# Performance work log

Hardware: AMD Instinct MI355X
Metric: run time of the kernel (lower is better)

The kernel has to match this reference:

```python
import jax, jax.numpy as jnp
import numpy as np


def _splat(img, sx, sy, w):
    """One bilinear-gaussian corner splat (scatter-add).
    img: (N,C,H,W); sx,sy,w: (N,1,H,W) integer-valued float shifts + weight.
    Returns (img_warp, one_warp) each (N,C,H,W).
    """
    N, C, H, W = img.shape
    ix = sx.astype(jnp.int32) + jnp.arange(H, dtype=jnp.int32)[None, None, :, None]
    iy = sy.astype(jnp.int32) + jnp.arange(W, dtype=jnp.int32)[None, None, None, :]
    mask = (ix >= 0) & (ix < H) & (iy >= 0) & (iy < W)          # (N,1,H,W)
    ixc = jnp.clip(ix, 0, H - 1)
    iyc = jnp.clip(iy, 0, W - 1)
    nb = jnp.arange(N, dtype=jnp.int32)[:, None, None, None]
    cb = jnp.arange(C, dtype=jnp.int32)[None, :, None, None]
    ids = ((nb * C + cb) * H + ixc) * W + iyc                   # (N,C,H,W)
    ids = jnp.broadcast_to(ids, (N, C, H, W)).reshape(-1)
    wv = jnp.where(mask, w, 0.0)                                # invalid -> 0 contribution
    vals = jnp.broadcast_to(img * wv, (N, C, H, W)).reshape(-1)
    wflat = jnp.broadcast_to(wv, (N, C, H, W)).reshape(-1)
    img_warp = jnp.zeros(N * C * H * W, img.dtype).at[ids].add(vals)
    one_warp = jnp.zeros(N * C * H * W, img.dtype).at[ids].add(wflat)
    return img_warp.reshape(N, C, H, W), one_warp.reshape(N, C, H, W)


def setup_inputs() -> dict:
    key = jax.random.key(0)
    k1, k2 = jax.random.split(key)
    N, C, H, W = 4, 128, 216, 384
    img = jax.random.normal(k1, (N, C, H, W), dtype=jnp.float32)
    # flow displacements of a few pixels magnitude (realistic optical flow)
    flo = jax.random.normal(k2, (N, 2, H, W), dtype=jnp.float32) * 8.0
    return {"img": img, "flo": flo}


def reference(img, flo):
    # y shifts rows (H axis), x shifts cols (W axis), matching the torch code
    y = flo[:, 0:1]    # (N,1,H,W)
    x = flo[:, 1:2]
    x1 = jnp.floor(x); x2 = x1 + 1.0
    y1 = jnp.floor(y); y2 = y1 + 1.0
    w11 = jnp.exp(-((x - x1) ** 2 + (y - y1) ** 2))
    w12 = jnp.exp(-((x - x1) ** 2 + (y - y2) ** 2))
    w21 = jnp.exp(-((x - x2) ** 2 + (y - y1) ** 2))
    w22 = jnp.exp(-((x - x2) ** 2 + (y - y2) ** 2))
    img11, o11 = _splat(img, x1, y1, w11)
    img12, o12 = _splat(img, x1, y2, w12)
    img21, o21 = _splat(img, x2, y1, w21)
    img22, o22 = _splat(img, x2, y2, w22)
    imgw = img11 + img12 + img21 + img22
    o = o11 + o12 + o21 + o22
    return imgw, o
```

## Files before the change

### kernel.cpp

```cpp
#include <hip/hip_runtime.h>


constexpr int N_ = 4, C_ = 128, H_ = 216, W_ = 384;
constexpr int HW    = H_ * W_;
constexpr int TOTAL = N_ * C_ * HW;
constexpr int PIX   = N_ * HW;
constexpr int SCAN_BLOCKS = PIX / 256;

constexpr size_t OFF_IMGT   = 0;
constexpr size_t OFF_OUTT   = (size_t)TOTAL;
constexpr size_t OFF_COUNTS = 2ull * TOTAL;
constexpr size_t OFF_CURSOR = OFF_COUNTS + PIX;
constexpr size_t OFF_OFFS   = OFF_CURSOR + PIX;
constexpr size_t OFF_BS     = OFF_OFFS + PIX;
constexpr size_t OFF_ONES   = OFF_BS + 4096;
constexpr size_t OFF_ES     = OFF_ONES + PIX;
constexpr size_t OFF_EW     = OFF_ES + 4ull * PIX;
constexpr size_t WS_ELEMS   = OFF_EW + 4ull * PIX;
constexpr size_t WS_BYTES   = WS_ELEMS * 4;

__device__ inline void corner_math(float fx, float fy, int& ifx, int& ify,
                                   float& ex0, float& ex1, float& ey0, float& ey1) {
    float fx1 = floorf(fx), fy1 = floorf(fy);
    float dx = fx - fx1, dy = fy - fy1;
    ifx = (int)fx1; ify = (int)fy1;
    ex0 = __expf(-dx * dx);
    ex1 = __expf(-(dx - 1.f) * (dx - 1.f));
    ey0 = __expf(-dy * dy);
    ey1 = __expf(-(dy - 1.f) * (dy - 1.f));
}

__global__ __launch_bounds__(256) void transpose_fwd_k(const float* __restrict__ img,
                                                       float* __restrict__ imgT) {
    __shared__ float tile[32][33];
    int n   = blockIdx.z;
    int hw0 = blockIdx.x * 32;
    int c0  = blockIdx.y * 32;
    const float* src = img  + (size_t)n * C_ * HW;
    float*       dst = imgT + (size_t)n * HW * C_;
    int tx = threadIdx.x, ty = threadIdx.y;
#pragma unroll
    for (int r = 0; r < 32; r += 8)
        tile[ty + r][tx] = src[(size_t)(c0 + ty + r) * HW + hw0 + tx];
    __syncthreads();
#pragma unroll
    for (int r = 0; r < 32; r += 8)
        dst[(size_t)(hw0 + ty + r) * C_ + c0 + tx] = tile[tx][ty + r];
}

__global__ __launch_bounds__(256) void count_k(const float* __restrict__ flo,
                                               unsigned int* __restrict__ counts) {
    int idx = blockIdx.x * 256 + threadIdx.x;
    if (idx >= PIX) return;
    int s = idx % HW, n = idx / HW;
    int h = s / W_, w = s % W_;
    float fy = flo[(n * 2 + 0) * HW + s];
    float fx = flo[(n * 2 + 1) * HW + s];
    int ifx, ify; float ex0, ex1, ey0, ey1;
    corner_math(fx, fy, ifx, ify, ex0, ex1, ey0, ey1);
    int ix = h + ifx, iy = w + ify;
    unsigned int* base = counts + (size_t)n * HW;
    bool bx0 = (unsigned)ix       < (unsigned)H_;
    bool bx1 = (unsigned)(ix + 1) < (unsigned)H_;
    bool by0 = (unsigned)iy       < (unsigned)W_;
    bool by1 = (unsigned)(iy + 1) < (unsigned)W_;
    if (bx0 && by0) atomicAdd(base + ix * W_ + iy, 1u);
    if (bx0 && by1) atomicAdd(base + ix * W_ + iy + 1, 1u);
    if (bx1 && by0) atomicAdd(base + (ix + 1) * W_ + iy, 1u);
    if (bx1 && by1) atomicAdd(base + (ix + 1) * W_ + iy + 1, 1u);
}

__global__ __launch_bounds__(256) void scan_local_k(const unsigned int* __restrict__ counts,
                                                    unsigned int* __restrict__ offs,
                                                    unsigned int* __restrict__ bs) {
    __shared__ unsigned int tmp[256];
    int tid = threadIdx.x;
    int i = blockIdx.x * 256 + tid;
    unsigned int v = counts[i];
    tmp[tid] = v;
    __syncthreads();
    for (int off = 1; off < 256; off <<= 1) {
        unsigned int t = (tid >= off) ? tmp[tid - off] : 0u;
        __syncthreads();
        tmp[tid] += t;
        __syncthreads();
    }
    offs[i] = tmp[tid] - v;
    if (tid == 255) bs[blockIdx.x] = tmp[tid];
}

__global__ __launch_bounds__(256) void scan_bs_k(unsigned int* __restrict__ bs) {
    __shared__ unsigned int tmp[256];
    constexpr int IT = 6;
    int tid = threadIdx.x;
    unsigned int v[IT]; unsigned int sum = 0;
#pragma unroll
    for (int i = 0; i < IT; ++i) {
        int j = tid * IT + i;
        v[i] = (j < SCAN_BLOCKS) ? bs[j] : 0u;
        sum += v[i];
    }
    tmp[tid] = sum;
    __syncthreads();
    for (int off = 1; off < 256; off <<= 1) {
        unsigned int t = (tid >= off) ? tmp[tid - off] : 0u;
        __syncthreads();
        tmp[tid] += t;
        __syncthreads();
    }
    unsigned int run = tmp[tid] - sum;
#pragma unroll
    for (int i = 0; i < IT; ++i) {
        int j = tid * IT + i;
        if (j < SCAN_BLOCKS) { unsigned int old = v[i]; bs[j] = run; run += old; }
    }
}

__global__ __launch_bounds__(256) void scan_add_k(unsigned int* __restrict__ offs,
                                                  const unsigned int* __restrict__ bs) {
    int i = blockIdx.x * 256 + threadIdx.x;
    offs[i] += bs[blockIdx.x];
}

__global__ __launch_bounds__(256) void fill_k(const float* __restrict__ flo,
                                              const unsigned int* __restrict__ offs,
                                              unsigned int* __restrict__ cursor,
                                              unsigned int* __restrict__ entry_s,
                                              float* __restrict__ entry_w) {
    int idx = blockIdx.x * 256 + threadIdx.x;
    if (idx >= PIX) return;
    int s = idx % HW, n = idx / HW;
    int h = s / W_, w = s % W_;
    float fy = flo[(n * 2 + 0) * HW + s];
    float fx = flo[(n * 2 + 1) * HW + s];
    int ifx, ify; float ex0, ex1, ey0, ey1;
    corner_math(fx, fy, ifx, ify, ex0, ex1, ey0, ey1);
    int ix = h + ifx, iy = w + ify;
    bool bx[2] = { (unsigned)ix < (unsigned)H_, (unsigned)(ix + 1) < (unsigned)H_ };
    bool by[2] = { (unsigned)iy < (unsigned)W_, (unsigned)(iy + 1) < (unsigned)W_ };
    float exw[2] = { ex0, ex1 }, eyw[2] = { ey0, ey1 };
#pragma unroll
    for (int a = 0; a < 2; ++a) {
#pragma unroll
        for (int b = 0; b < 2; ++b) {
            if (bx[a] && by[b]) {
                int t = n * HW + (ix + a) * W_ + (iy + b);
                unsigned int slot = atomicAdd(cursor + t, 1u);
                unsigned int e = offs[t] + slot;
                entry_s[e] = (unsigned int)s;
                entry_w[e] = exw[a] * eyw[b];
            }
        }
    }
}

__global__ __launch_bounds__(256) void gather_k(const float* __restrict__ imgT,
                                                const unsigned int* __restrict__ counts,
                                                const unsigned int* __restrict__ offs,
                                                const unsigned int* __restrict__ entry_s,
                                                const float* __restrict__ entry_w,
                                                float* __restrict__ outT,
                                                float* __restrict__ ones_plane) {
    int pl = threadIdx.x >> 5;
    int cg = threadIdx.x & 31;
    int t  = blockIdx.x * 8 + pl;
    int n = t / HW, p = t % HW;
    unsigned int k   = counts[t];
    unsigned int off = offs[t];
    float4 acc = make_float4(0.f, 0.f, 0.f, 0.f);
    float wsum = 0.f;
    const float4* srcBase = (const float4*)(imgT + (size_t)n * HW * C_);
    for (unsigned int j = 0; j < k; ++j) {
        unsigned int s = entry_s[off + j];
        float wgt     = entry_w[off + j];
        float4 v = srcBase[(size_t)s * (C_ / 4) + cg];
        acc.x += wgt * v.x; acc.y += wgt * v.y;
        acc.z += wgt * v.z; acc.w += wgt * v.w;
        wsum += wgt;
    }
    ((float4*)(outT + ((size_t)n * HW + p) * C_))[cg] = acc;
    if (cg == 0) ones_plane[t] = wsum;
}

__global__ __launch_bounds__(256) void transpose_back_k(const float* __restrict__ outT,
                                                        float* __restrict__ out) {
    __shared__ float tile[32][33];
    int n   = blockIdx.z;
    int hw0 = blockIdx.x * 32;
    int c0  = blockIdx.y * 32;
    const float* src = outT + (size_t)n * HW * C_;
    float*       dst = out  + (size_t)n * C_ * HW;
    int tx = threadIdx.x, ty = threadIdx.y;
#pragma unroll
    for (int r = 0; r < 32; r += 8)
        tile[ty + r][tx] = src[(size_t)(hw0 + ty + r) * C_ + c0 + tx];
    __syncthreads();
#pragma unroll
    for (int r = 0; r < 32; r += 8)
        dst[(size_t)(c0 + ty + r) * HW + hw0 + tx] = tile[tx][ty + r];
}

__global__ __launch_bounds__(256) void ones_bcast_k(const float* __restrict__ ones_plane,
                                                    float* __restrict__ out_ones) {
    constexpr int HW4 = HW / 4;
    int idx = blockIdx.x * 256 + threadIdx.x;
    int p  = idx % HW4;
    int cn = idx / HW4;
    int c  = cn % C_;
    int n  = cn / C_;
    const float4* src = (const float4*)(ones_plane + (size_t)n * HW);
    float4*       dst = (float4*)(out_ones + ((size_t)n * C_ + c) * HW);
    dst[p] = src[p];
}

__global__ __launch_bounds__(256) void fb_ones_scatter_k(const float* __restrict__ flo,
                                                         float* __restrict__ out_ones) {
    int idx = blockIdx.x * 256 + threadIdx.x;
    if (idx >= PIX) return;
    int w = idx % W_; int hn = idx / W_; int h = hn % H_; int n = hn / H_;
    float fy = flo[(n * 2 + 0) * HW + h * W_ + w];
    float fx = flo[(n * 2 + 1) * HW + h * W_ + w];
    int ifx, ify; float ex0, ex1, ey0, ey1;
    corner_math(fx, fy, ifx, ify, ex0, ex1, ey0, ey1);
    int ix = h + ifx, iy = w + ify;
    float* plane = out_ones + (size_t)n * C_ * HW;
    if ((unsigned)ix < (unsigned)H_ && (unsigned)iy < (unsigned)W_) atomicAdd(plane + ix * W_ + iy, ex0 * ey0);
    if ((unsigned)ix < (unsigned)H_ && (unsigned)(iy+1) < (unsigned)W_) atomicAdd(plane + ix * W_ + iy + 1, ex0 * ey1);
    if ((unsigned)(ix+1) < (unsigned)H_ && (unsigned)iy < (unsigned)W_) atomicAdd(plane + (ix+1) * W_ + iy, ex1 * ey0);
    if ((unsigned)(ix+1) < (unsigned)H_ && (unsigned)(iy+1) < (unsigned)W_) atomicAdd(plane + (ix+1) * W_ + iy + 1, ex1 * ey1);
}

__global__ __launch_bounds__(256) void fb_img_scatter_k(const float* __restrict__ img,
                                                        const float* __restrict__ flo,
                                                        float* __restrict__ out_img) {
    int idx = blockIdx.x * 256 + threadIdx.x;
    if (idx >= TOTAL) return;
    int w = idx % W_; int rem = idx / W_; int h = rem % H_; rem /= H_;
    int c = rem % C_; int n = rem / C_;
    float fy = flo[(n * 2 + 0) * HW + h * W_ + w];
    float fx = flo[(n * 2 + 1) * HW + h * W_ + w];
    int ifx, ify; float ex0, ex1, ey0, ey1;
    corner_math(fx, fy, ifx, ify, ex0, ex1, ey0, ey1);
    int ix = h + ifx, iy = w + ify;
    float v = img[idx];
    float* plane = out_img + (size_t)(n * C_ + c) * HW;
    if ((unsigned)ix < (unsigned)H_ && (unsigned)iy < (unsigned)W_) atomicAdd(plane + ix * W_ + iy, v * ex0 * ey0);
    if ((unsigned)ix < (unsigned)H_ && (unsigned)(iy+1) < (unsigned)W_) atomicAdd(plane + ix * W_ + iy + 1, v * ex0 * ey1);
    if ((unsigned)(ix+1) < (unsigned)H_ && (unsigned)iy < (unsigned)W_) atomicAdd(plane + (ix+1) * W_ + iy, v * ex1 * ey0);
    if ((unsigned)(ix+1) < (unsigned)H_ && (unsigned)(iy+1) < (unsigned)W_) atomicAdd(plane + (ix+1) * W_ + iy + 1, v * ex1 * ey1);
}

__global__ __launch_bounds__(256) void fb_ones_bcast_k(float* __restrict__ out_ones) {
    constexpr int HW4 = HW / 4;
    constexpr int TOT = N_ * (C_ - 1) * HW4;
    int idx = blockIdx.x * 256 + threadIdx.x;
    if (idx >= TOT) return;
    int p = idx % HW4; int cn = idx / HW4;
    int c = 1 + cn % (C_ - 1); int n = cn / (C_ - 1);
    const float4* src = (const float4*)(out_ones + (size_t)n * C_ * HW);
    float4*       dst = (float4*)(out_ones + ((size_t)n * C_ + c) * HW);
    dst[p] = src[p];
}

extern "C" void kernel_launch(void* const* d_in, const int* in_sizes, int n_in,
                              void* d_out, int out_size, void* d_ws, size_t ws_size,
                              hipStream_t stream) {
    const float* img = (const float*)d_in[0];
    const float* flo = (const float*)d_in[1];
    float* out      = (float*)d_out;
    float* out_img  = out;
    float* out_ones = out + (size_t)TOTAL;

    if (ws_size < WS_BYTES) {
        hipMemsetAsync(out_img, 0, (size_t)TOTAL * sizeof(float), stream);
        for (int n = 0; n < N_; ++n)
            hipMemsetAsync(out_ones + (size_t)n * C_ * HW, 0, HW * sizeof(float), stream);
        fb_ones_scatter_k<<<(PIX + 255) / 256, 256, 0, stream>>>(flo, out_ones);
        fb_img_scatter_k<<<(TOTAL + 255) / 256, 256, 0, stream>>>(img, flo, out_img);
        fb_ones_bcast_k<<<(N_ * (C_ - 1) * (HW / 4) + 255) / 256, 256, 0, stream>>>(out_ones);
        return;
    }

    float* ws = (float*)d_ws;
    float*        imgT    = ws + OFF_IMGT;
    float*        outT    = ws + OFF_OUTT;
    unsigned int* counts  = (unsigned int*)(ws + OFF_COUNTS);
    unsigned int* cursor  = (unsigned int*)(ws + OFF_CURSOR);
    unsigned int* offs    = (unsigned int*)(ws + OFF_OFFS);
    unsigned int* bs      = (unsigned int*)(ws + OFF_BS);
    float*        ones_pl = ws + OFF_ONES;
    unsigned int* entry_s = (unsigned int*)(ws + OFF_ES);
    float*        entry_w = ws + OFF_EW;

    hipMemsetAsync(counts, 0, 2ull * PIX * sizeof(unsigned int), stream);

    dim3 tb(32, 8);
    transpose_fwd_k<<<dim3(HW / 32, C_ / 32, N_), tb, 0, stream>>>(img, imgT);
    count_k<<<SCAN_BLOCKS, 256, 0, stream>>>(flo, counts);
    scan_local_k<<<SCAN_BLOCKS, 256, 0, stream>>>(counts, offs, bs);
    scan_bs_k<<<1, 256, 0, stream>>>(bs);
    scan_add_k<<<SCAN_BLOCKS, 256, 0, stream>>>(offs, bs);
    fill_k<<<SCAN_BLOCKS, 256, 0, stream>>>(flo, offs, cursor, entry_s, entry_w);
    gather_k<<<PIX / 8, 256, 0, stream>>>(imgT, counts, offs, entry_s, entry_w, outT, ones_pl);
    transpose_back_k<<<dim3(HW / 32, C_ / 32, N_), tb, 0, stream>>>(outT, out_img);
    ones_bcast_k<<<(N_ * C_ * (HW / 4) + 255) / 256, 256, 0, stream>>>(ones_pl, out_ones);
}
```

Measured before the change: 778.1 us.

## Fuse gather with transpose-back and ones broadcast, pack entries, drop scan-add

The gather kernel now handles 64-pixel tiles. It accumulates channel-major results in registers, transposes them through an XOR-swizzled LDS tile, and writes the NCHW image output and the broadcast ones output directly. This removes the outT intermediate buffer, the transpose-back kernel and the ones broadcast kernel. Entry index and weight are packed into one uint2 array. The scan-add pass is folded into the consumers, which add the block sum on the fly. The gather loop is unrolled by two. The cost is a large 32 KB LDS tile per block, which may limit occupancy, plus higher register pressure from holding 8 float4 accumulators.

```diff
diff --git a/kernel.cpp b/kernel.cpp
--- a/kernel.cpp
+++ b/kernel.cpp
@@ -6,17 +6,16 @@
 constexpr int TOTAL = N_ * C_ * HW;
 constexpr int PIX   = N_ * HW;
 constexpr int SCAN_BLOCKS = PIX / 256;
+constexpr int PTILE = 64;
+constexpr int GATHER_BLOCKS = PIX / PTILE;
 
 constexpr size_t OFF_IMGT   = 0;
-constexpr size_t OFF_OUTT   = (size_t)TOTAL;
-constexpr size_t OFF_COUNTS = 2ull * TOTAL;
+constexpr size_t OFF_COUNTS = (size_t)TOTAL;
 constexpr size_t OFF_CURSOR = OFF_COUNTS + PIX;
 constexpr size_t OFF_OFFS   = OFF_CURSOR + PIX;
 constexpr size_t OFF_BS     = OFF_OFFS + PIX;
-constexpr size_t OFF_ONES   = OFF_BS + 4096;
-constexpr size_t OFF_ES     = OFF_ONES + PIX;
-constexpr size_t OFF_EW     = OFF_ES + 4ull * PIX;
-constexpr size_t WS_ELEMS   = OFF_EW + 4ull * PIX;
+constexpr size_t OFF_ENT    = OFF_BS + 4096;
+constexpr size_t WS_ELEMS   = OFF_ENT + 8ull * PIX;
 constexpr size_t WS_BYTES   = WS_ELEMS * 4;
 
 __device__ inline void corner_math(float fx, float fy, int& ifx, int& ify,
@@ -116,17 +115,11 @@
     }
 }
 
-__global__ __launch_bounds__(256) void scan_add_k(unsigned int* __restrict__ offs,
-                                                  const unsigned int* __restrict__ bs) {
-    int i = blockIdx.x * 256 + threadIdx.x;
-    offs[i] += bs[blockIdx.x];
-}
-
 __global__ __launch_bounds__(256) void fill_k(const float* __restrict__ flo,
                                               const unsigned int* __restrict__ offs,
+                                              const unsigned int* __restrict__ bs,
                                               unsigned int* __restrict__ cursor,
-                                              unsigned int* __restrict__ entry_s,
-                                              float* __restrict__ entry_w) {
+                                              uint2* __restrict__ entries) {
     int idx = blockIdx.x * 256 + threadIdx.x;
     if (idx >= PIX) return;
     int s = idx % HW, n = idx / HW;
@@ -146,71 +139,94 @@
             if (bx[a] && by[b]) {
                 int t = n * HW + (ix + a) * W_ + (iy + b);
                 unsigned int slot = atomicAdd(cursor + t, 1u);
-                unsigned int e = offs[t] + slot;
-                entry_s[e] = (unsigned int)s;
-                entry_w[e] = exw[a] * eyw[b];
+                unsigned int e = offs[t] + bs[t >> 8] + slot;
+                entries[e] = make_uint2((unsigned int)s,
+                                        __float_as_uint(exw[a] * eyw[b]));
             }
         }
     }
 }
 
-__global__ __launch_bounds__(256) void gather_k(const float* __restrict__ imgT,
-                                                const unsigned int* __restrict__ counts,
-                                                const unsigned int* __restrict__ offs,
-                                                const unsigned int* __restrict__ entry_s,
-                                                const float* __restrict__ entry_w,
-                                                float* __restrict__ outT,
-                                                float* __restrict__ ones_plane) {
-    int pl = threadIdx.x >> 5;
-    int cg = threadIdx.x & 31;
-    int t  = blockIdx.x * 8 + pl;
-    int n = t / HW, p = t % HW;
-    unsigned int k   = counts[t];
-    unsigned int off = offs[t];
-    float4 acc = make_float4(0.f, 0.f, 0.f, 0.f);
-    float wsum = 0.f;
+__global__ __launch_bounds__(256) void gather_fused_k(const float* __restrict__ imgT,
+                                                      const unsigned int* __restrict__ counts,
+                                                      const unsigned int* __restrict__ offs,
+                                                      const unsigned int* __restrict__ bs,
+                                                      const uint2* __restrict__ entries,
+                                                      float* __restrict__ out_img,
+                                                      float* __restrict__ out_ones) {
+    __shared__ float tile[C_ * PTILE];
+    __shared__ float wsum_lds[PTILE];
+
+    int tid = threadIdx.x;
+    int pl  = tid >> 5;
+    int cg  = tid & 31;
+    int bt  = blockIdx.x;
+    int n   = bt / (HW / PTILE);
+    int p0  = (bt % (HW / PTILE)) * PTILE;
     const float4* srcBase = (const float4*)(imgT + (size_t)n * HW * C_);
-    for (unsigned int j = 0; j < k; ++j) {
-        unsigned int s = entry_s[off + j];
-        float wgt     = entry_w[off + j];
-        float4 v = srcBase[(size_t)s * (C_ / 4) + cg];
-        acc.x += wgt * v.x; acc.y += wgt * v.y;
-        acc.z += wgt * v.z; acc.w += wgt * v.w;
-        wsum += wgt;
-    }
-    ((float4*)(outT + ((size_t)n * HW + p) * C_))[cg] = acc;
-    if (cg == 0) ones_plane[t] = wsum;
-}
-
-__global__ __launch_bounds__(256) void transpose_back_k(const float* __restrict__ outT,
-                                                        float* __restrict__ out) {
-    __shared__ float tile[32][33];
-    int n   = blockIdx.z;
-    int hw0 = blockIdx.x * 32;
-    int c0  = blockIdx.y * 32;
-    const float* src = outT + (size_t)n * HW * C_;
-    float*       dst = out  + (size_t)n * C_ * HW;
-    int tx = threadIdx.x, ty = threadIdx.y;
-#pragma unroll
-    for (int r = 0; r < 32; r += 8)
-        tile[ty + r][tx] = src[(size_t)(hw0 + ty + r) * C_ + c0 + tx];
+
+    float4 acc[8];
+    float  ws[8];
+#pragma unroll
+    for (int si = 0; si < 8; ++si) {
+        int p = si * 8 + pl;
+        int t = n * HW + p0 + p;
+        unsigned int k   = counts[t];
+        unsigned int off = offs[t] + bs[t >> 8];
+        float4 a = make_float4(0.f, 0.f, 0.f, 0.f);
+        float  w_s = 0.f;
+        unsigned int j = 0;
+        for (; j + 2 <= k; j += 2) {
+            uint2 e0 = entries[off + j];
+            uint2 e1 = entries[off + j + 1];
+            float w0 = __uint_as_float(e0.y);
+            float w1 = __uint_as_float(e1.y);
+            float4 v0 = srcBase[(size_t)e0.x * (C_ / 4) + cg];
+            float4 v1 = srcBase[(size_t)e1.x * (C_ / 4) + cg];
+            a.x = a.x + w0 * v0.x + w1 * v1.x;
+            a.y = a.y + w0 * v0.y + w1 * v1.y;
+            a.z = a.z + w0 * v0.z + w1 * v1.z;
+            a.w = a.w + w0 * v0.w + w1 * v1.w;
+            w_s = w_s + w0 + w1;
+        }
+        if (j < k) {
+            uint2 e0 = entries[off + j];
+            float w0 = __uint_as_float(e0.y);
+            float4 v0 = srcBase[(size_t)e0.x * (C_ / 4) + cg];
+            a.x += w0 * v0.x; a.y += w0 * v0.y;
+            a.z += w0 * v0.z; a.w += w0 * v0.w;
+            w_s += w0;
+        }
+        acc[si] = a; ws[si] = w_s;
+    }
+
+#pragma unroll
+    for (int si = 0; si < 8; ++si) {
+        int p  = si * 8 + pl;
+        if (cg == 0) wsum_lds[p] = ws[si];
+        int p4 = p >> 2, pr = p & 3;
+        float av[4] = { acc[si].x, acc[si].y, acc[si].z, acc[si].w };
+#pragma unroll
+        for (int jj = 0; jj < 4; ++jj) {
+            int c    = 4 * cg + jj;
+            int slot = p4 ^ ((c >> 2) & 15);
+            tile[c * PTILE + slot * 4 + pr] = av[jj];
+        }
+    }
     __syncthreads();
-#pragma unroll
-    for (int r = 0; r < 32; r += 8)
-        dst[(size_t)(c0 + ty + r) * HW + hw0 + tx] = tile[tx][ty + r];
-}
-
-__global__ __launch_bounds__(256) void ones_bcast_k(const float* __restrict__ ones_plane,
-                                                    float* __restrict__ out_ones) {
-    constexpr int HW4 = HW / 4;
-    int idx = blockIdx.x * 256 + threadIdx.x;
-    int p  = idx % HW4;
-    int cn = idx / HW4;
-    int c  = cn % C_;
-    int n  = cn / C_;
-    const float4* src = (const float4*)(ones_plane + (size_t)n * HW);
-    float4*       dst = (float4*)(out_ones + ((size_t)n * C_ + c) * HW);
-    dst[p] = src[p];
+
+    int p4    = tid & 15;
+    int cbase = tid >> 4;
+    float4 wv = ((const float4*)wsum_lds)[p4];
+#pragma unroll
+    for (int i = 0; i < 8; ++i) {
+        int c    = cbase + 16 * i;
+        int slot = p4 ^ ((c >> 2) & 15);
+        float4 v = *(const float4*)&tile[c * PTILE + slot * 4];
+        size_t o = ((size_t)(n * C_ + c)) * HW + p0 + p4 * 4;
+        *(float4*)(out_img  + o) = v;
+        *(float4*)(out_ones + o) = wv;
+    }
 }
 
 __global__ __launch_bounds__(256) void fb_ones_scatter_k(const float* __restrict__ flo,
@@ -283,14 +299,11 @@
 
     float* ws = (float*)d_ws;
     float*        imgT    = ws + OFF_IMGT;
-    float*        outT    = ws + OFF_OUTT;
     unsigned int* counts  = (unsigned int*)(ws + OFF_COUNTS);
     unsigned int* cursor  = (unsigned int*)(ws + OFF_CURSOR);
     unsigned int* offs    = (unsigned int*)(ws + OFF_OFFS);
     unsigned int* bs      = (unsigned int*)(ws + OFF_BS);
-    float*        ones_pl = ws + OFF_ONES;
-    unsigned int* entry_s = (unsigned int*)(ws + OFF_ES);
-    float*        entry_w = ws + OFF_EW;
+    uint2*        entries = (uint2*)(ws + OFF_ENT);
 
     hipMemsetAsync(counts, 0, 2ull * PIX * sizeof(unsigned int), stream);
 
@@ -299,9 +312,7 @@
     count_k<<<SCAN_BLOCKS, 256, 0, stream>>>(flo, counts);
     scan_local_k<<<SCAN_BLOCKS, 256, 0, stream>>>(counts, offs, bs);
     scan_bs_k<<<1, 256, 0, stream>>>(bs);
-    scan_add_k<<<SCAN_BLOCKS, 256, 0, stream>>>(offs, bs);
-    fill_k<<<SCAN_BLOCKS, 256, 0, stream>>>(flo, offs, cursor, entry_s, entry_w);
-    gather_k<<<PIX / 8, 256, 0, stream>>>(imgT, counts, offs, entry_s, entry_w, outT, ones_pl);
-    transpose_back_k<<<dim3(HW / 32, C_ / 32, N_), tb, 0, stream>>>(outT, out_img);
-    ones_bcast_k<<<(N_ * C_ * (HW / 4) + 255) / 256, 256, 0, stream>>>(ones_pl, out_ones);
-}
+    fill_k<<<SCAN_BLOCKS, 256, 0, stream>>>(flo, offs, bs, cursor, entries);
+    gather_fused_k<<<GATHER_BLOCKS, 256, 0, stream>>>(imgT, counts, offs, bs,
+                                                      entries, out_img, out_ones);
+}
```

Measured after the change: 762.6 us. 1.02x faster.
